# Kernel optimization log

Measured on AMD Instinct MI355X. Metric: run time of the kernel, lower is better.

## Reference

```python
import jax, jax.numpy as jnp
import numpy as np
import math

B, S, D, H, DK = 2, 4096, 512, 8, 64

def setup_inputs() -> dict:
    key = jax.random.key(0)
    ks = jax.random.split(key, 11)
    scale = 1.0 / math.sqrt(D)
    inp = {
        'q': jax.random.normal(ks[0], (B, S, D), jnp.float32),
        'k': jax.random.normal(ks[1], (B, S, D), jnp.float32),
        'v': jax.random.normal(ks[2], (B, S, D), jnp.float32),
        # causal mask: True = masked (as consumed by masked_fill)
        'mask': jnp.triu(jnp.ones((S, S), jnp.bool_), k=1)[None, None, :, :],
        'wq': jax.random.normal(ks[3], (D, D), jnp.float32) * scale,
        'bq': jnp.zeros((D,), jnp.float32),
        'wk': jax.random.normal(ks[4], (D, D), jnp.float32) * scale,
        'bk': jnp.zeros((D,), jnp.float32),
        'wv': jax.random.normal(ks[5], (D, D), jnp.float32) * scale,
        'bv': jnp.zeros((D,), jnp.float32),
        'wo': jax.random.normal(ks[6], (D, D), jnp.float32) * scale,
        'bo': jnp.zeros((D,), jnp.float32),
    }
    return inp

def reference(q, k, v, mask, wq, bq, wk, bk, wv, bv, wo, bo):
    # torch nn.Linear: y = x @ W^T + b
    def proj(x, w, b):
        return x @ w.T + b
    def heads(x):  # [B,S,D] -> [B,H,S,DK]
        return x.reshape(B, S, H, DK).transpose(0, 2, 1, 3)
    qh = heads(proj(q, wq, bq))
    kh = heads(proj(k, wk, bk))
    vh = heads(proj(v, wv, bv))
    scores = jnp.einsum('bhqd,bhkd->bhqk', qh, kh) / math.sqrt(DK)
    # NOTE: faithful to source, masked positions are filled with -1e-09 (not -inf)
    scores = jnp.where(mask, jnp.float32(-1e-09), scores)
    attn = jax.nn.softmax(scores, axis=-1)
    x = jnp.einsum('bhqk,bhkd->bhqd', attn, vh)
    x = x.transpose(0, 2, 1, 3).reshape(B, S, D)
    return proj(x, wo, bo)
```

## Files before the change

### kernel.cpp

```cpp
#include <hip/hip_runtime.h>
#include <math.h>

#define SS 4096
#define DD 512
#define HH 8
#define DKK 64

#define MSUB 4.0f
#define W_MASK 0.0183156393f

typedef _Float16 half8_t __attribute__((ext_vector_type(8)));
typedef _Float16 half4_t __attribute__((ext_vector_type(4)));
typedef float f32x4 __attribute__((ext_vector_type(4)));
typedef float f32x16 __attribute__((ext_vector_type(16)));

__device__ __forceinline__ f32x4 mfma16(half8_t a, half8_t b, f32x4 c) {
    return __builtin_amdgcn_mfma_f32_16x16x32_f16(a, b, c, 0, 0, 0);
}
__device__ __forceinline__ f32x16 mfma32(half8_t a, half8_t b, f32x16 c) {
    return __builtin_amdgcn_mfma_f32_32x32x16_f16(a, b, c, 0, 0, 0);
}
__device__ __forceinline__ f32x16 zero16() {
    f32x16 z;
#pragma unroll
    for (int i = 0; i < 16; i++) z[i] = 0.f;
    return z;
}
__device__ __forceinline__ void gld_lds16(const _Float16* g, _Float16* l) {
    __builtin_amdgcn_global_load_lds((const __attribute__((address_space(1))) void*)g,
                                     (__attribute__((address_space(3))) void*)l, 16, 0, 0);
}

__global__ __launch_bounds__(256) void cvt_prep(
    const float* __restrict__ q, const float* __restrict__ k, const float* __restrict__ v,
    const float* __restrict__ wq, const float* __restrict__ wk,
    const float* __restrict__ wv, const float* __restrict__ wo,
    _Float16* qf, _Float16* kf, _Float16* vf,
    _Float16* wqf, _Float16* wkf, _Float16* wvf, _Float16* wof)
{
    const float* srcs[7] = {q, k, v, wq, wk, wv, wo};
    _Float16* dsts[7] = {qf, kf, vf, wqf, wkf, wvf, wof};
    const int ns[7] = {4194304, 4194304, 4194304, 262144, 262144, 262144, 262144};
    int t = blockIdx.y;
    size_t i0 = ((size_t)blockIdx.x * 256 + threadIdx.x) * 8;
    if (i0 >= (size_t)ns[t]) return;
    const float* s = srcs[t];
    _Float16* d = dsts[t];
    float4 a = *(const float4*)(s + i0);
    float4 b = *(const float4*)(s + i0 + 4);
    half8_t h = {(_Float16)a.x, (_Float16)a.y, (_Float16)a.z, (_Float16)a.w,
                 (_Float16)b.x, (_Float16)b.y, (_Float16)b.z, (_Float16)b.w};
    *(half8_t*)(d + i0) = h;
}

__global__ __launch_bounds__(256, 3) void gemm_qkv(
    const _Float16* __restrict__ qf, const _Float16* __restrict__ kf,
    const _Float16* __restrict__ vf,
    const _Float16* __restrict__ wqf, const _Float16* __restrict__ wkf,
    const _Float16* __restrict__ wvf,
    const float* __restrict__ bq, const float* __restrict__ bk,
    const float* __restrict__ bv,
    _Float16* __restrict__ Qf, _Float16* __restrict__ Kf,
    _Float16* __restrict__ Vf, _Float16* __restrict__ Vt)
{
    __shared__ __align__(16) _Float16 smem[16384];
    const int z = blockIdx.z;
    const _Float16* A = z == 0 ? qf : (z == 1 ? kf : vf);
    const _Float16* W = z == 0 ? wqf : (z == 1 ? wkf : wvf);
    const float* bias = z == 0 ? bq : (z == 1 ? bk : bv);

    const int tid = threadIdx.x;
    const int w = tid >> 6, lane = tid & 63, q = lane >> 4, cc = lane & 15;
    const int mtile = blockIdx.x * 128, ntile = blockIdx.y * 128;
    const int mw = (w & 1) * 64, nw = (w >> 1) * 64;
    const int srow = lane >> 3, scol = (lane & 7) * 8;

    f32x4 acc[4][4];
#pragma unroll
    for (int i = 0; i < 4; i++)
#pragma unroll
        for (int j = 0; j < 4; j++) {
            f32x4 zf = {0.f, 0.f, 0.f, 0.f};
            acc[i][j] = zf;
        }

    for (int kt = 0; kt < 512; kt += 64) {
        __syncthreads();
#pragma unroll
        for (int i = 0; i < 4; i++) {
            int r0 = w * 32 + i * 8;
            gld_lds16(A + (size_t)(mtile + r0 + srow) * 512 + kt + scol, &smem[r0 * 64]);
            gld_lds16(W + (size_t)(ntile + r0 + srow) * 512 + kt + scol, &smem[8192 + r0 * 64]);
        }
        __syncthreads();
#pragma unroll
        for (int kh = 0; kh < 2; kh++) {
            half8_t ar[4], br[4];
#pragma unroll
            for (int i = 0; i < 4; i++)
                ar[i] = *(const half8_t*)(&smem[(mw + i * 16 + cc) * 64 + kh * 32 + q * 8]);
#pragma unroll
            for (int j = 0; j < 4; j++)
                br[j] = *(const half8_t*)(&smem[8192 + (nw + j * 16 + cc) * 64 + kh * 32 + q * 8]);
#pragma unroll
            for (int i = 0; i < 4; i++)
#pragma unroll
                for (int j = 0; j < 4; j++)
                    acc[i][j] = mfma16(ar[i], br[j], acc[i][j]);
        }
    }

#pragma unroll
    for (int jb = 0; jb < 4; jb++) {
        int n = ntile + nw + jb * 16 + cc;
        float bvv = bias[n];
        int h = n >> 6, dkl = n & 63;
#pragma unroll
        for (int it = 0; it < 4; it++) {
            int m0 = mtile + mw + it * 16 + q * 4;
            int b = m0 >> 12;
            int sq0 = m0 & 4095;
            int bh = b * 8 + h;
            if (z == 0) {
#pragma unroll
                for (int r = 0; r < 4; r++) {
                    int sq = sq0 + r;
                    size_t addr = ((size_t)(bh * 128 + (sq >> 5)) * 4 + (dkl >> 4)) * 512
                                  + ((sq & 31) + 32 * ((dkl >> 3) & 1)) * 8 + (dkl & 7);
                    Qf[addr] = (_Float16)(acc[it][jb][r] + bvv);
                }
            } else if (z == 1) {
#pragma unroll
                for (int r = 0; r < 4; r++) {
                    int sq = sq0 + r;
                    size_t addr = ((size_t)(bh * 64 + (sq >> 6)) * 8
                                   + ((sq >> 5) & 1) * 4 + (dkl >> 4)) * 512
                                  + ((sq & 31) + 32 * ((dkl >> 3) & 1)) * 8 + (dkl & 7);
                    Kf[addr] = (_Float16)(acc[it][jb][r] + bvv);
                }
            } else {
                half4_t pk;
#pragma unroll
                for (int r = 0; r < 4; r++) {
                    int sq = sq0 + r;
                    float val = acc[it][jb][r] + bvv;
                    pk[r] = (_Float16)val;
                    size_t addr = ((size_t)(bh * 64 + (sq >> 6)) * 8
                                   + ((sq >> 4) & 3) * 2 + (dkl >> 5)) * 512
                                  + ((dkl & 31) + 32 * ((sq >> 2) & 1)) * 8
                                  + ((sq & 3) + 4 * ((sq >> 3) & 1));
                    Vf[addr] = (_Float16)val;
                }
                *(half4_t*)(Vt + ((size_t)bh * 64 + dkl) * SS + sq0) = pk;
            }
        }
    }
}

__global__ __launch_bounds__(256) void suffix_v(const _Float16* __restrict__ Vt,
                                                _Float16* __restrict__ SufVt)
{
    __shared__ float csum[4][65];
    const int bh = blockIdx.x >> 4;
    const int dk = (blockIdx.x & 15) * 4 + (threadIdx.x >> 6);
    const int dki = threadIdx.x >> 6;
    const int c = threadIdx.x & 63;
    const _Float16* vp = Vt + ((size_t)bh * 64 + dk) * SS + c * 64;

    half8_t v8[8];
    float acc = 0.f;
#pragma unroll
    for (int j = 0; j < 8; j++) {
        v8[j] = *(const half8_t*)(vp + j * 8);
#pragma unroll
        for (int t = 0; t < 8; t++) acc += (float)v8[j][t];
    }
    csum[dki][c] = acc;
    __syncthreads();
    if (threadIdx.x < 4) {
        float a = 0.f;
        for (int c2 = 63; c2 >= 0; c2--) {
            float t2 = csum[threadIdx.x][c2];
            csum[threadIdx.x][c2] = a;
            a += t2;
        }
    }
    __syncthreads();
    float a = csum[dki][c];
    _Float16* op = SufVt + ((size_t)bh * 64 + dk) * SS + c * 64;
#pragma unroll
    for (int j = 7; j >= 0; j--) {
        half8_t o8;
#pragma unroll
        for (int t = 7; t >= 0; t--) {
            o8[t] = (_Float16)a;
            a += (float)v8[j][t];
        }
        *(half8_t*)(op + j * 8) = o8;
    }
}

__device__ __forceinline__ void exp_pack(const f32x16& s, half8_t& pa, half8_t& pb,
                                         float& lsum) {
#pragma unroll
    for (int i = 0; i < 16; i++) {
        float p = __expf(fmaf(s[i], 0.125f, -MSUB));
        lsum += p;
        if (i < 8) pa[i] = (_Float16)p; else pb[i - 8] = (_Float16)p;
    }
}
__device__ __forceinline__ void exp_pack_mask(const f32x16& s, int j0, int mg, int h5,
                                              half8_t& pa, half8_t& pb, float& lsum) {
#pragma unroll
    for (int i = 0; i < 16; i++) {
        int jg = j0 + (i & 3) + 8 * (i >> 2) + 4 * h5;
        float p = __expf(fmaf(s[i], 0.125f, -MSUB));
        if (jg > mg) p = 0.f;
        lsum += p;
        if (i < 8) pa[i] = (_Float16)p; else pb[i - 8] = (_Float16)p;
    }
}

__global__ __launch_bounds__(256, 2) void attn_kernel(
    const _Float16* __restrict__ Qf, const _Float16* __restrict__ Kf,
    const _Float16* __restrict__ Vf, const _Float16* __restrict__ SufVt,
    _Float16* __restrict__ X)
{
    const int tid = threadIdx.x;
    const int w = tid >> 6, lane = tid & 63;
    const int h5 = lane >> 5, l31 = lane & 31;
    const int bh = blockIdx.x & 15;
    const int seg = blockIdx.x >> 4;
    const int wp = w >> 1;
    const int qg = ((w & 1) == 0) ? (seg * 2 + wp) : (127 - seg * 2 - wp);

    const int qbase = qg * 32;
    const int jdiag = qbase & ~63;
    const int jsd = (qbase >> 5) & 1;
    const int mg = qbase + l31;

    const _Float16* qp = Qf + (size_t)(bh * 128 + (qbase >> 5)) * 4 * 512 + lane * 8;
    half8_t qfr[4];
#pragma unroll
    for (int s = 0; s < 4; s++) qfr[s] = *(const half8_t*)(qp + s * 512);

    const _Float16* Kb = Kf + (size_t)bh * 64 * 4096 + lane * 8;
    const _Float16* Vb = Vf + (size_t)bh * 64 * 4096 + lane * 8;

    f32x16 o0 = zero16(), o1 = zero16();
    float lsum = 0.f;

    const int nfull = jdiag >> 6;
    for (int jblk = 0; jblk < nfull; jblk++) {
        const _Float16* kg = Kb + (size_t)jblk * 4096;
        const _Float16* vg = Vb + (size_t)jblk * 4096;
        f32x16 sa = zero16(), sb = zero16();
#pragma unroll
        for (int s = 0; s < 4; s++)
            sa = mfma32(*(const half8_t*)(kg + s * 512), qfr[s], sa);
#pragma unroll
        for (int s = 0; s < 4; s++)
            sb = mfma32(*(const half8_t*)(kg + (4 + s) * 512), qfr[s], sb);
        half8_t p0a, p0b, p1a, p1b;
        exp_pack(sa, p0a, p0b, lsum);
        exp_pack(sb, p1a, p1b, lsum);
        o0 = mfma32(p0a, *(const half8_t*)(vg + 0 * 512), o0);
        o1 = mfma32(p0a, *(const half8_t*)(vg + 1 * 512), o1);
        o0 = mfma32(p0b, *(const half8_t*)(vg + 2 * 512), o0);
        o1 = mfma32(p0b, *(const half8_t*)(vg + 3 * 512), o1);
        o0 = mfma32(p1a, *(const half8_t*)(vg + 4 * 512), o0);
        o1 = mfma32(p1a, *(const half8_t*)(vg + 5 * 512), o1);
        o0 = mfma32(p1b, *(const half8_t*)(vg + 6 * 512), o0);
        o1 = mfma32(p1b, *(const half8_t*)(vg + 7 * 512), o1);
    }

    {
        const _Float16* kg = Kb + (size_t)nfull * 4096;
        const _Float16* vg = Vb + (size_t)nfull * 4096;
        f32x16 sa = zero16();
#pragma unroll
        for (int s = 0; s < 4; s++)
            sa = mfma32(*(const half8_t*)(kg + s * 512), qfr[s], sa);
        half8_t p0a, p0b;
        if (jsd == 0) exp_pack_mask(sa, jdiag, mg, h5, p0a, p0b, lsum);
        else          exp_pack(sa, p0a, p0b, lsum);
        o0 = mfma32(p0a, *(const half8_t*)(vg + 0 * 512), o0);
        o1 = mfma32(p0a, *(const half8_t*)(vg + 1 * 512), o1);
        o0 = mfma32(p0b, *(const half8_t*)(vg + 2 * 512), o0);
        o1 = mfma32(p0b, *(const half8_t*)(vg + 3 * 512), o1);
        if (jsd == 1) {
            f32x16 sb = zero16();
#pragma unroll
            for (int s = 0; s < 4; s++)
                sb = mfma32(*(const half8_t*)(kg + (4 + s) * 512), qfr[s], sb);
            half8_t p1a, p1b;
            exp_pack_mask(sb, jdiag + 32, mg, h5, p1a, p1b, lsum);
            o0 = mfma32(p1a, *(const half8_t*)(vg + 4 * 512), o0);
            o1 = mfma32(p1a, *(const half8_t*)(vg + 5 * 512), o1);
            o0 = mfma32(p1b, *(const half8_t*)(vg + 6 * 512), o0);
            o1 = mfma32(p1b, *(const half8_t*)(vg + 7 * 512), o1);
        }
    }

    lsum += __shfl_xor(lsum, 32);

    const int b = bh >> 3, hh = bh & 7;
#pragma unroll
    for (int r = 0; r < 16; r++) {
        int ml = (r & 3) + 8 * (r >> 2) + 4 * h5;
        float lv = __shfl(lsum, ml);
        int s = qbase + ml;
        float iv = 1.f / (lv + (float)(SS - 1 - s) * W_MASK);
        float sv0 = (float)SufVt[((size_t)bh * 64 + l31) * SS + s];
        float sv1 = (float)SufVt[((size_t)bh * 64 + 32 + l31) * SS + s];
        X[((size_t)b * SS + s) * DD + hh * 64 + l31] =
            (_Float16)((o0[r] + W_MASK * sv0) * iv);
        X[((size_t)b * SS + s) * DD + hh * 64 + 32 + l31] =
            (_Float16)((o1[r] + W_MASK * sv1) * iv);
    }
}

__global__ __launch_bounds__(256, 4) void gemm_out(
    const _Float16* __restrict__ A, const _Float16* __restrict__ W,
    const float* __restrict__ bias, float* __restrict__ Cout)
{
    __shared__ __align__(16) _Float16 smem[12288];
    const int tid = threadIdx.x;
    const int w = tid >> 6, lane = tid & 63, q = lane >> 4, cc = lane & 15;
    const int mtile = blockIdx.x * 128, ntile = blockIdx.y * 64;
    const int mw = (w & 1) * 64, nw = (w >> 1) * 32;
    const int srow = lane >> 3, scol = (lane & 7) * 8;

    f32x4 acc[4][2];
#pragma unroll
    for (int i = 0; i < 4; i++)
#pragma unroll
        for (int j = 0; j < 2; j++) {
            f32x4 zf = {0.f, 0.f, 0.f, 0.f};
            acc[i][j] = zf;
        }

    for (int kt = 0; kt < 512; kt += 64) {
        __syncthreads();
#pragma unroll
        for (int i = 0; i < 4; i++) {
            int r0 = w * 32 + i * 8;
            gld_lds16(A + (size_t)(mtile + r0 + srow) * 512 + kt + scol, &smem[r0 * 64]);
        }
#pragma unroll
        for (int i = 0; i < 2; i++) {
            int r0 = w * 16 + i * 8;
            gld_lds16(W + (size_t)(ntile + r0 + srow) * 512 + kt + scol, &smem[8192 + r0 * 64]);
        }
        __syncthreads();
#pragma unroll
        for (int kh = 0; kh < 2; kh++) {
            half8_t ar[4], br[2];
#pragma unroll
            for (int i = 0; i < 4; i++)
                ar[i] = *(const half8_t*)(&smem[(mw + i * 16 + cc) * 64 + kh * 32 + q * 8]);
#pragma unroll
            for (int j = 0; j < 2; j++)
                br[j] = *(const half8_t*)(&smem[8192 + (nw + j * 16 + cc) * 64 + kh * 32 + q * 8]);
#pragma unroll
            for (int i = 0; i < 4; i++)
#pragma unroll
                for (int j = 0; j < 2; j++)
                    acc[i][j] = mfma16(ar[i], br[j], acc[i][j]);
        }
    }

#pragma unroll
    for (int j = 0; j < 2; j++) {
        int coln = ntile + nw + j * 16 + cc;
        float bvv = bias[coln];
#pragma unroll
        for (int i = 0; i < 4; i++) {
            int m0 = mtile + mw + i * 16 + q * 4;
#pragma unroll
            for (int r = 0; r < 4; r++)
                Cout[(size_t)(m0 + r) * 512 + coln] = acc[i][j][r] + bvv;
        }
    }
}

extern "C" void kernel_launch(void* const* d_in, const int* in_sizes, int n_in,
                              void* d_out, int out_size, void* d_ws, size_t ws_size,
                              hipStream_t stream) {
    const float* q  = (const float*)d_in[0];
    const float* k  = (const float*)d_in[1];
    const float* v  = (const float*)d_in[2];
    const float* wq = (const float*)d_in[4];
    const float* bq = (const float*)d_in[5];
    const float* wk = (const float*)d_in[6];
    const float* bk = (const float*)d_in[7];
    const float* wv = (const float*)d_in[8];
    const float* bv = (const float*)d_in[9];
    const float* wo = (const float*)d_in[10];
    const float* bo = (const float*)d_in[11];
    float* out = (float*)d_out;

    char* ws = (char*)d_ws;
    const size_t MB = (size_t)1024 * 1024;
    _Float16* qf  = (_Float16*)(ws);
    _Float16* kf  = (_Float16*)(ws + 8 * MB);
    _Float16* vf  = (_Float16*)(ws + 16 * MB);
    _Float16* wqf = (_Float16*)(ws + 24 * MB);
    _Float16* wkf = (_Float16*)(ws + 24 * MB + 512 * 1024);
    _Float16* wvf = (_Float16*)(ws + 25 * MB);
    _Float16* wof = (_Float16*)(ws + 25 * MB + 512 * 1024);
    _Float16* Qfr = (_Float16*)(ws + 26 * MB);
    _Float16* Kfr = (_Float16*)(ws + 34 * MB);
    _Float16* Vfr = (_Float16*)(ws + 42 * MB);
    _Float16* Vt  = (_Float16*)(ws + 50 * MB);
    _Float16* SufVt = qf;
    _Float16* Xa    = kf;

    hipLaunchKernelGGL(cvt_prep, dim3(2048, 7), dim3(256), 0, stream,
                       q, k, v, wq, wk, wv, wo, qf, kf, vf, wqf, wkf, wvf, wof);
    hipLaunchKernelGGL(gemm_qkv, dim3(64, 4, 3), dim3(256), 0, stream,
                       qf, kf, vf, wqf, wkf, wvf, bq, bk, bv, Qfr, Kfr, Vfr, Vt);
    hipLaunchKernelGGL(suffix_v, dim3(256), dim3(256), 0, stream, Vt, SufVt);
    hipLaunchKernelGGL(attn_kernel, dim3(512), dim3(256), 0, stream,
                       Qfr, Kfr, Vfr, SufVt, Xa);
    hipLaunchKernelGGL(gemm_out, dim3(64, 8), dim3(256), 0, stream, Xa, wof, bo, out);
}
```

Baseline: 265.1 us.

## Split attention KV range across two waves with reduce kernel; stage QKV epilogue in LDS

The attention kernel now runs one 32-row query tile per 128-thread block, with its two waves each handling half of the key blocks. Partial outputs and row sums go to global buffers, and a new attn_reduce kernel combines them, applies the mask correction and normalizes. This is meant to raise parallelism and balance the causal workload without the earlier paired-tile scheme, at the cost of an extra launch and partial-result traffic. The QKV GEMM epilogue also stages results through padded shared memory so the fragment-layout stores can be 16-byte vectors instead of scattered 2-byte writes.

Result: slower. 314.9 us (+18.8%).

```diff
diff --git a/kernel.cpp b/kernel.cpp
--- a/kernel.cpp
+++ b/kernel.cpp
@@ -8,6 +8,7 @@
 
 #define MSUB 4.0f
 #define W_MASK 0.0183156393f
+#define CST 136
 
 typedef _Float16 half8_t __attribute__((ext_vector_type(8)));
 typedef _Float16 half4_t __attribute__((ext_vector_type(4)));
@@ -63,7 +64,7 @@
     _Float16* __restrict__ Qf, _Float16* __restrict__ Kf,
     _Float16* __restrict__ Vf, _Float16* __restrict__ Vt)
 {
-    __shared__ __align__(16) _Float16 smem[16384];
+    __shared__ __align__(16) _Float16 smem[17408];
     const int z = blockIdx.z;
     const _Float16* A = z == 0 ? qf : (z == 1 ? kf : vf);
     const _Float16* W = z == 0 ? wqf : (z == 1 ? wkf : wvf);
@@ -71,6 +72,7 @@
 
     const int tid = threadIdx.x;
     const int w = tid >> 6, lane = tid & 63, q = lane >> 4, cc = lane & 15;
+    const int h5 = lane >> 5, l31 = lane & 31;
     const int mtile = blockIdx.x * 128, ntile = blockIdx.y * 128;
     const int mw = (w & 1) * 64, nw = (w >> 1) * 64;
     const int srow = lane >> 3, scol = (lane & 7) * 8;
@@ -110,49 +112,73 @@
         }
     }
 
+    const int b = mtile >> 12;
+    const int ms = mtile & 4095;
+
+    __syncthreads();
 #pragma unroll
     for (int jb = 0; jb < 4; jb++) {
-        int n = ntile + nw + jb * 16 + cc;
+        int nloc = nw + jb * 16 + cc;
+        int n = ntile + nloc;
         float bvv = bias[n];
-        int h = n >> 6, dkl = n & 63;
 #pragma unroll
         for (int it = 0; it < 4; it++) {
-            int m0 = mtile + mw + it * 16 + q * 4;
-            int b = m0 >> 12;
-            int sq0 = m0 & 4095;
-            int bh = b * 8 + h;
-            if (z == 0) {
-#pragma unroll
-                for (int r = 0; r < 4; r++) {
-                    int sq = sq0 + r;
-                    size_t addr = ((size_t)(bh * 128 + (sq >> 5)) * 4 + (dkl >> 4)) * 512
-                                  + ((sq & 31) + 32 * ((dkl >> 3) & 1)) * 8 + (dkl & 7);
-                    Qf[addr] = (_Float16)(acc[it][jb][r] + bvv);
-                }
-            } else if (z == 1) {
-#pragma unroll
-                for (int r = 0; r < 4; r++) {
-                    int sq = sq0 + r;
-                    size_t addr = ((size_t)(bh * 64 + (sq >> 6)) * 8
-                                   + ((sq >> 5) & 1) * 4 + (dkl >> 4)) * 512
-                                  + ((sq & 31) + 32 * ((dkl >> 3) & 1)) * 8 + (dkl & 7);
-                    Kf[addr] = (_Float16)(acc[it][jb][r] + bvv);
-                }
-            } else {
-                half4_t pk;
-#pragma unroll
-                for (int r = 0; r < 4; r++) {
-                    int sq = sq0 + r;
-                    float val = acc[it][jb][r] + bvv;
-                    pk[r] = (_Float16)val;
-                    size_t addr = ((size_t)(bh * 64 + (sq >> 6)) * 8
-                                   + ((sq >> 4) & 3) * 2 + (dkl >> 5)) * 512
-                                  + ((dkl & 31) + 32 * ((sq >> 2) & 1)) * 8
-                                  + ((sq & 3) + 4 * ((sq >> 3) & 1));
-                    Vf[addr] = (_Float16)val;
-                }
-                *(half4_t*)(Vt + ((size_t)bh * 64 + dkl) * SS + sq0) = pk;
+            int mloc = mw + it * 16 + q * 4;
+            half4_t pk;
+#pragma unroll
+            for (int r = 0; r < 4; r++) {
+                _Float16 hv = (_Float16)(acc[it][jb][r] + bvv);
+                pk[r] = hv;
+                smem[(mloc + r) * CST + nloc] = hv;
             }
+            if (z == 2) {
+                int bh = b * 8 + (n >> 6);
+                int dkl = n & 63;
+                *(half4_t*)(Vt + ((size_t)bh * 64 + dkl) * SS + ms + mloc) = pk;
+            }
+        }
+    }
+    __syncthreads();
+
+    if (z == 0) {
+#pragma unroll
+        for (int i = 0; i < 8; i++) {
+            int e = w * 8 + i;
+            int s5 = e >> 3, hh = (e >> 2) & 1, d4 = e & 3;
+            int row = s5 * 32 + l31;
+            int col = hh * 64 + d4 * 16 + h5 * 8;
+            half8_t vv = *(const half8_t*)(&smem[row * CST + col]);
+            int bh = b * 8 + (ntile >> 6) + hh;
+            size_t base = ((size_t)(bh * 128 + (ms >> 5) + s5) * 4 + d4) * 512;
+            *(half8_t*)(Qf + base + lane * 8) = vv;
+        }
+    } else if (z == 1) {
+#pragma unroll
+        for (int i = 0; i < 8; i++) {
+            int e = w * 8 + i;
+            int s6 = e >> 4, s5b = (e >> 3) & 1, hh = (e >> 2) & 1, d4 = e & 3;
+            int row = s6 * 64 + s5b * 32 + l31;
+            int col = hh * 64 + d4 * 16 + h5 * 8;
+            half8_t vv = *(const half8_t*)(&smem[row * CST + col]);
+            int bh = b * 8 + (ntile >> 6) + hh;
+            size_t base = ((size_t)(bh * 64 + (ms >> 6) + s6) * 8 + s5b * 4 + d4) * 512;
+            *(half8_t*)(Kf + base + lane * 8) = vv;
+        }
+    } else {
+#pragma unroll
+        for (int i = 0; i < 8; i++) {
+            int e = w * 8 + i;
+            int s6 = e >> 4, c = (e >> 2) & 3, hh = (e >> 1) & 1, d5 = e & 1;
+            int col = hh * 64 + d5 * 32 + l31;
+            half8_t vv;
+#pragma unroll
+            for (int k0 = 0; k0 < 8; k0++) {
+                int mrow = s6 * 64 + c * 16 + (k0 & 3) + 4 * h5 + 8 * (k0 >> 2);
+                vv[k0] = smem[mrow * CST + col];
+            }
+            int bh = b * 8 + (ntile >> 6) + hh;
+            size_t base = ((size_t)(bh * 64 + (ms >> 6) + s6) * 8 + c * 2 + d5) * 512;
+            *(half8_t*)(Vf + base + lane * 8) = vv;
         }
     }
 }
@@ -221,23 +247,23 @@
     }
 }
 
-__global__ __launch_bounds__(256, 2) void attn_kernel(
+__global__ __launch_bounds__(128) void attn_part(
     const _Float16* __restrict__ Qf, const _Float16* __restrict__ Kf,
-    const _Float16* __restrict__ Vf, const _Float16* __restrict__ SufVt,
-    _Float16* __restrict__ X)
+    const _Float16* __restrict__ Vf,
+    _Float16* __restrict__ Op0, _Float16* __restrict__ Op1,
+    float* __restrict__ Lpart)
 {
     const int tid = threadIdx.x;
     const int w = tid >> 6, lane = tid & 63;
     const int h5 = lane >> 5, l31 = lane & 31;
     const int bh = blockIdx.x & 15;
-    const int seg = blockIdx.x >> 4;
-    const int wp = w >> 1;
-    const int qg = ((w & 1) == 0) ? (seg * 2 + wp) : (127 - seg * 2 - wp);
-
+    const int qg = 127 - (int)(blockIdx.x >> 4);
     const int qbase = qg * 32;
     const int jdiag = qbase & ~63;
     const int jsd = (qbase >> 5) & 1;
     const int mg = qbase + l31;
+    const int nfull = jdiag >> 6;
+    const int T2 = (nfull + 1) >> 1;
 
     const _Float16* qp = Qf + (size_t)(bh * 128 + (qbase >> 5)) * 4 * 512 + lane * 8;
     half8_t qfr[4];
@@ -250,8 +276,9 @@
     f32x16 o0 = zero16(), o1 = zero16();
     float lsum = 0.f;
 
-    const int nfull = jdiag >> 6;
-    for (int jblk = 0; jblk < nfull; jblk++) {
+    const int lo = (w == 0) ? 0 : T2;
+    const int hi = (w == 0) ? T2 : nfull;
+    for (int jblk = lo; jblk < hi; jblk++) {
         const _Float16* kg = Kb + (size_t)jblk * 4096;
         const _Float16* vg = Vb + (size_t)jblk * 4096;
         f32x16 sa = zero16(), sb = zero16();
@@ -274,7 +301,7 @@
         o1 = mfma32(p1b, *(const half8_t*)(vg + 7 * 512), o1);
     }
 
-    {
+    if (w == 1) {
         const _Float16* kg = Kb + (size_t)nfull * 4096;
         const _Float16* vg = Vb + (size_t)nfull * 4096;
         f32x16 sa = zero16();
@@ -302,21 +329,55 @@
         }
     }
 
-    lsum += __shfl_xor(lsum, 32);
+    const size_t task = (size_t)bh * 128 + qg;
+    _Float16* Opw = (w == 0 ? Op0 : Op1) + task * 2048;
+    Lpart[(task * 2 + w) * 64 + lane] = lsum;
+#pragma unroll
+    for (int r = 0; r < 16; r++) {
+        int row = (r & 3) + 8 * (r >> 2) + 4 * h5;
+        Opw[row * 64 + l31] = (_Float16)o0[r];
+        Opw[row * 64 + 32 + l31] = (_Float16)o1[r];
+    }
+}
+
+__global__ __launch_bounds__(256) void attn_reduce(
+    const _Float16* __restrict__ Op0, const _Float16* __restrict__ Op1,
+    const float* __restrict__ Lpart, const _Float16* __restrict__ SufVt,
+    _Float16* __restrict__ X)
+{
+    __shared__ _Float16 sfv[32 * 64];
+    __shared__ float linv[32];
+    const int t = threadIdx.x;
+    const int bh = blockIdx.x & 15;
+    const int qg = blockIdx.x >> 4;
+    const int qbase = qg * 32;
+    const size_t task = (size_t)bh * 128 + qg;
+
+#pragma unroll
+    for (int i = 0; i < 8; i++) {
+        int dk = i * 8 + (t >> 5);
+        int sl = t & 31;
+        sfv[sl * 64 + dk] = SufVt[((size_t)bh * 64 + dk) * SS + qbase + sl];
+    }
+    if (t < 32) {
+        const float* lp = Lpart + task * 128;
+        float l = lp[t] + lp[t + 32] + lp[64 + t] + lp[64 + t + 32];
+        linv[t] = 1.f / (l + (float)(SS - 1 - qbase - t) * W_MASK);
+    }
+    __syncthreads();
 
     const int b = bh >> 3, hh = bh & 7;
-#pragma unroll
-    for (int r = 0; r < 16; r++) {
-        int ml = (r & 3) + 8 * (r >> 2) + 4 * h5;
-        float lv = __shfl(lsum, ml);
-        int s = qbase + ml;
-        float iv = 1.f / (lv + (float)(SS - 1 - s) * W_MASK);
-        float sv0 = (float)SufVt[((size_t)bh * 64 + l31) * SS + s];
-        float sv1 = (float)SufVt[((size_t)bh * 64 + 32 + l31) * SS + s];
-        X[((size_t)b * SS + s) * DD + hh * 64 + l31] =
-            (_Float16)((o0[r] + W_MASK * sv0) * iv);
-        X[((size_t)b * SS + s) * DD + hh * 64 + 32 + l31] =
-            (_Float16)((o1[r] + W_MASK * sv1) * iv);
+    const int dk = t & 63;
+    const int r0 = t >> 6;
+    const _Float16* oa = Op0 + task * 2048;
+    const _Float16* ob = Op1 + task * 2048;
+#pragma unroll
+    for (int i = 0; i < 8; i++) {
+        int r = r0 + 4 * i;
+        float o = (float)oa[r * 64 + dk] + (float)ob[r * 64 + dk];
+        float val = (o + W_MASK * (float)sfv[r * 64 + dk]) * linv[r];
+        int s = qbase + r;
+        X[((size_t)b * SS + s) * DD + hh * 64 + dk] = (_Float16)val;
     }
 }
 
@@ -413,15 +474,20 @@
     _Float16* Kfr = (_Float16*)(ws + 34 * MB);
     _Float16* Vfr = (_Float16*)(ws + 42 * MB);
     _Float16* Vt  = (_Float16*)(ws + 50 * MB);
+    float*    Lp  = (float*)(ws + 58 * MB);
     _Float16* SufVt = qf;
     _Float16* Xa    = kf;
+    _Float16* Op0   = vf;
+    _Float16* Op1   = Vt;
 
     hipLaunchKernelGGL(cvt_prep, dim3(2048, 7), dim3(256), 0, stream,
                        q, k, v, wq, wk, wv, wo, qf, kf, vf, wqf, wkf, wvf, wof);
     hipLaunchKernelGGL(gemm_qkv, dim3(64, 4, 3), dim3(256), 0, stream,
                        qf, kf, vf, wqf, wkf, wvf, bq, bk, bv, Qfr, Kfr, Vfr, Vt);
     hipLaunchKernelGGL(suffix_v, dim3(256), dim3(256), 0, stream, Vt, SufVt);
-    hipLaunchKernelGGL(attn_kernel, dim3(512), dim3(256), 0, stream,
-                       Qfr, Kfr, Vfr, SufVt, Xa);
+    hipLaunchKernelGGL(attn_part, dim3(2048), dim3(128), 0, stream,
+                       Qfr, Kfr, Vfr, Op0, Op1, Lp);
+    hipLaunchKernelGGL(attn_reduce, dim3(2048), dim3(256), 0, stream,
+                       Op0, Op1, Lp, SufVt, Xa);
     hipLaunchKernelGGL(gemm_out, dim3(64, 8), dim3(256), 0, stream, Xa, wof, bo, out);
 }
```
